# Kernel optimization log

Hardware: AMD Instinct MI355X
Metric: run time of the kernel (lower is better)

The kernel has to match this reference:

```python
import jax, jax.numpy as jnp
import numpy as np

D_MODEL, D_K, D_V, HEADS = 512, 8, 8, 6
EPS = 1e-5


def setup_inputs() -> dict:
    key = jax.random.key(0)
    ks = jax.random.split(key, 16)
    B, S = 16, 1024
    inp = {
        'q_input': jax.random.normal(ks[0], (B, S, D_MODEL), jnp.float32),
        'k_input': jax.random.normal(ks[1], (B, S, D_MODEL), jnp.float32),
        'v_input': jax.random.normal(ks[2], (B, S, D_MODEL), jnp.float32),
        'mask': jax.random.randint(ks[3], (B, S, S), 0, 2).astype(bool),
        'Wq': jax.random.normal(ks[4], (D_MODEL, D_K * HEADS), jnp.float32) * 0.04,
        'bq': jax.random.normal(ks[5], (D_K * HEADS,), jnp.float32) * 0.02,
        'Wk': jax.random.normal(ks[6], (D_MODEL, D_K * HEADS), jnp.float32) * 0.04,
        'bk': jax.random.normal(ks[7], (D_K * HEADS,), jnp.float32) * 0.02,
        'Wv': jax.random.normal(ks[8], (D_MODEL, D_V * HEADS), jnp.float32) * 0.04,
        'bv': jax.random.normal(ks[9], (D_V * HEADS,), jnp.float32) * 0.02,
        'Wo': jax.random.normal(ks[10], (HEADS * D_K, D_MODEL), jnp.float32) * 0.1,
        'bo': jax.random.normal(ks[11], (D_MODEL,), jnp.float32) * 0.02,
        'ln_w': 1.0 + jax.random.normal(ks[12], (D_MODEL,), jnp.float32) * 0.02,
        'ln_b': jax.random.normal(ks[13], (D_MODEL,), jnp.float32) * 0.02,
    }
    return inp


def reference(q_input, k_input, v_input, mask, Wq, bq, Wk, bk, Wv, bv, Wo, bo, ln_w, ln_b):
    B, S, _ = q_input.shape
    # projections -> [B, H, S, d]
    q_s = (q_input @ Wq + bq).reshape(B, S, HEADS, D_K).transpose(0, 2, 1, 3)
    k_s = (k_input @ Wk + bk).reshape(B, S, HEADS, D_K).transpose(0, 2, 1, 3)
    v_s = (v_input @ Wv + bv).reshape(B, S, HEADS, D_V).transpose(0, 2, 1, 3)
    # scaled dot-product with masked_fill(mask, 1e-9) as in the original (fills VALUE, not -inf)
    scores = jnp.einsum('bhqd,bhkd->bhqk', q_s, k_s) / np.sqrt(D_K).astype(np.float32)
    scores = jnp.where(mask[:, None, :, :], jnp.float32(1e-9), scores)
    attn = jax.nn.softmax(scores, axis=-1)
    out = jnp.einsum('bhqk,bhkd->bhqd', attn, v_s)  # [B,H,S,d_v]
    out = out.transpose(0, 2, 1, 3).reshape(B, S, HEADS * D_K)
    out = out @ Wo + bo
    x = q_input + out  # residual
    mu = jnp.mean(x, axis=-1, keepdims=True)
    var = jnp.var(x, axis=-1, keepdims=True)
    return (x - mu) * jax.lax.rsqrt(var + EPS) * ln_w + ln_b
```

## Files before the change

### kernel.cpp

```cpp
#include <hip/hip_runtime.h>

constexpr int B = 16;
constexpr int S = 1024;
constexpr int DM = 512;
constexpr int H = 6;
constexpr int DK = 8;
constexpr int NJ = H * DK;
constexpr int BS = B * S;
constexpr int WB_ELEMS = 16 * NJ * 32;

typedef __attribute__((ext_vector_type(8))) short bf16x8;
typedef __attribute__((ext_vector_type(8))) _Float16 half8;
typedef __attribute__((ext_vector_type(4))) _Float16 half4;
typedef __attribute__((ext_vector_type(4))) float floatx4;

#define LOG2E 1.4426950408889634f
#define QSCALE (0.35355339059327373f * LOG2E)

__device__ inline ushort f2bf(float f) {
  unsigned int u = __builtin_bit_cast(unsigned int, f);
  return (ushort)((u + 0x7FFFu + ((u >> 16) & 1u)) >> 16);
}

__global__ __launch_bounds__(256) void maskbits_kernel(
    const int* __restrict__ mask, unsigned long long* __restrict__ bits) {
  int wave = threadIdx.x >> 6, lane = threadIdx.x & 63;
  int row = blockIdx.x * 4 + wave;
  const int* mrow = mask + (size_t)row * S;
  unsigned long long* brow = bits + (size_t)row * 16;
  int koff = ((lane >> 5) << 5) + 2 * (lane & 15) + ((lane >> 4) & 1);
#pragma unroll
  for (int c = 0; c < 16; c++) {
    int v = mrow[c * 64 + koff];
    unsigned long long bal = __ballot(v != 0);
    if (lane == 0) brow[c] = bal;
  }
}

__global__ __launch_bounds__(256) void wprep_kernel(
    const float* __restrict__ Wq, const float* __restrict__ Wk,
    const float* __restrict__ Wv, ushort* __restrict__ Wb,
    uint2* __restrict__ VBf) {
  int m = blockIdx.x;
  if (m < 3) {
    const float* W = (m == 0) ? Wq : (m == 1) ? Wk : Wv;
    ushort* dst = Wb + (size_t)m * WB_ELEMS;
    for (int e = threadIdx.x; e < WB_ELEMS; e += 256) {
      int kc = e / 1536;
      int rem = e - kc * 1536;
      int n = rem >> 5, kj = rem & 31;
      dst[e] = f2bf(W[(size_t)(kc * 32 + kj) * NJ + n]);
    }
  } else {
    int bh = m - 3;
    for (int i = threadIdx.x; i < 2048; i += 256) {
      int tile = i >> 5;
      int li = i & 31;
      int g = li >> 3, dd = 8 + (li & 7);
      uint hv = (dd == 8) ? 0x3C003C00u : 0u;
      uint2 val; val.x = hv; val.y = hv;
      VBf[((size_t)bh * 64 + tile) * 64 + g * 16 + dd] = val;
    }
  }
}

__global__ __launch_bounds__(256) void proj_kernel(
    const float* __restrict__ q_in, const float* __restrict__ k_in,
    const float* __restrict__ v_in, const ushort* __restrict__ Wb,
    const float* __restrict__ bq, const float* __restrict__ bk,
    const float* __restrict__ bv,
    ushort* __restrict__ Qo, ushort* __restrict__ Ko, ushort* __restrict__ Vo) {
  int m = blockIdx.y;
  const float* x    = (m == 0) ? q_in : (m == 1) ? k_in : v_in;
  const float* bias = (m == 0) ? bq   : (m == 1) ? bk   : bv;
  ushort* out       = (m == 0) ? Qo   : (m == 1) ? Ko   : Vo;
  float oscale      = (m == 0) ? QSCALE : 1.0f;
  const ushort* Wg  = Wb + (size_t)m * WB_ELEMS;

  __shared__ ushort Wl[WB_ELEMS];

  int t = threadIdx.x;
  int r0 = blockIdx.x * 64;
  int wave = t >> 6, lane = t & 63;
  int n16 = lane & 15, quad = lane >> 4;
  const float* xrow = x + (size_t)(r0 + wave * 16 + n16) * DM + quad * 8;

  float4 pa[4], pb[4];
#pragma unroll
  for (int i = 0; i < 4; i++) {
    pa[i] = *(const float4*)(xrow + i * 32);
    pb[i] = *(const float4*)(xrow + i * 32 + 4);
  }

  {
    const uint4* src = (const uint4*)Wg;
    uint4* dst = (uint4*)Wl;
#pragma unroll
    for (int i = 0; i < 12; i++) dst[t + i * 256] = src[t + i * 256];
  }

  floatx4 acc0 = {0.f, 0.f, 0.f, 0.f};
  floatx4 acc1 = {0.f, 0.f, 0.f, 0.f};
  floatx4 acc2 = {0.f, 0.f, 0.f, 0.f};

  __syncthreads();

#pragma unroll
  for (int kc = 0; kc < 16; kc++) {
    float4 xa = pa[kc & 3];
    float4 xb = pb[kc & 3];
    if (kc + 4 < 16) {
      pa[kc & 3] = *(const float4*)(xrow + (kc + 4) * 32);
      pb[kc & 3] = *(const float4*)(xrow + (kc + 4) * 32 + 4);
    }
    bf16x8 a;
    a[0] = (short)f2bf(xa.x); a[1] = (short)f2bf(xa.y);
    a[2] = (short)f2bf(xa.z); a[3] = (short)f2bf(xa.w);
    a[4] = (short)f2bf(xb.x); a[5] = (short)f2bf(xb.y);
    a[6] = (short)f2bf(xb.z); a[7] = (short)f2bf(xb.w);
    const ushort* wbase = &Wl[(kc * 48 + n16) * 32 + quad * 8];
    bf16x8 b0 = *(const bf16x8*)(wbase);
    bf16x8 b1 = *(const bf16x8*)(wbase + 16 * 32);
    bf16x8 b2 = *(const bf16x8*)(wbase + 32 * 32);
    acc0 = __builtin_amdgcn_mfma_f32_16x16x32_bf16(a, b0, acc0, 0, 0, 0);
    acc1 = __builtin_amdgcn_mfma_f32_16x16x32_bf16(a, b1, acc1, 0, 0, 0);
    acc2 = __builtin_amdgcn_mfma_f32_16x16x32_bf16(a, b2, acc2, 0, 0, 0);
  }

  int baseR = r0 + wave * 16 + quad * 4;
#pragma unroll
  for (int j = 0; j < 3; j++) {
    floatx4 a = (j == 0) ? acc0 : (j == 1) ? acc1 : acc2;
    int n = j * 16 + n16;
    float bn = bias[n];
    int h = n >> 3, d = n & 7;
#pragma unroll
    for (int r = 0; r < 4; r++) {
      int R = baseR + r;
      int b = R >> 10, s = R & 1023;
      float fv = (a[r] + bn) * oscale;
      if (m == 2) {
        size_t idx =
            ((((size_t)(b * H + h) * 64 + (s >> 4)) * 64) +
             ((s >> 2) & 3) * 16 + d) * 4 + (s & 3);
        out[idx] = __builtin_bit_cast(ushort, (_Float16)fv);
      } else {
        out[(((size_t)(b * H + h)) * S + s) * 8 + d] = f2bf(fv);
      }
    }
  }
}

__global__ __launch_bounds__(256, 3) void attn_kernel(
    const ushort* __restrict__ Qg, const ushort* __restrict__ Kg,
    const ushort* __restrict__ VBg ,
    const uint* __restrict__ bits32, float* __restrict__ A) {
  int bh = blockIdx.x >> 4;
  int qt = blockIdx.x & 15;
  int b = bh / H, h = bh % H;
  int q0 = qt * 64;

  __shared__ uint4 Kl[1024];
  __shared__ uint2 Vl[64 * 64];

  int t = threadIdx.x;
  int wave = t >> 6, lane = t & 63;
  int quad = lane >> 4, n16 = lane & 15;

  {
    const uint4* Ksrc = (const uint4*)(Kg + (size_t)bh * S * 8);
#pragma unroll
    for (int i = 0; i < 4; i++) Kl[t + i * 256] = Ksrc[t + i * 256];
    const uint2* Vsrc = (const uint2*)VBg + (size_t)bh * (64 * 64);
#pragma unroll
    for (int i = 0; i < 16; i++) Vl[t + i * 256] = Vsrc[t + i * 256];
  }

  bf16x8 aq = {0, 0, 0, 0, 0, 0, 0, 0};
  if (quad == 0)
    aq = *(const bf16x8*)&Qg[((size_t)bh * S + q0 + wave * 16 + n16) * 8];

  const uint* mrow = bits32 + (size_t)(b * S + q0 + wave * 16 + n16) * 32;

  __syncthreads();

  floatx4 acc0 = {0.f, 0.f, 0.f, 0.f};
  floatx4 acc1 = {0.f, 0.f, 0.f, 0.f};
  const floatx4 zero = {0.f, 0.f, 0.f, 0.f};
  int sh0 = 2 * quad;

  const ushort* kb = (const ushort*)Kl + n16 * 8;
  const uint2* vbb = Vl + lane;

#pragma unroll
  for (int cc = 0; cc < 8; cc++) {
    uint4 mq = *(const uint4*)(mrow + cc * 4);
#pragma unroll
    for (int ci = 0; ci < 4; ci++) {
      int c = cc * 4 + ci;
      uint mw = (ci == 0) ? mq.x : (ci == 1) ? mq.y : (ci == 2) ? mq.z : mq.w;

      bf16x8 ak0 = *(const bf16x8*)(kb + c * 256);
      bf16x8 ak1 = *(const bf16x8*)(kb + c * 256 + 128);
      uint2 vb0 = vbb[(2 * c) * 64];
      uint2 vb1 = vbb[(2 * c + 1) * 64];

      floatx4 s0 = __builtin_amdgcn_mfma_f32_16x16x32_bf16(ak0, aq, zero, 0, 0, 0);
      floatx4 s1 = __builtin_amdgcn_mfma_f32_16x16x32_bf16(ak1, aq, zero, 0, 0, 0);

      float p0 = exp2f(fminf(s0[0], 15.f)), p1 = exp2f(fminf(s0[1], 15.f));
      float p2 = exp2f(fminf(s0[2], 15.f)), p3 = exp2f(fminf(s0[3], 15.f));
      float p4 = exp2f(fminf(s1[0], 15.f)), p5 = exp2f(fminf(s1[1], 15.f));
      float p6 = exp2f(fminf(s1[2], 15.f)), p7 = exp2f(fminf(s1[3], 15.f));
      uint w0 = __builtin_bit_cast(uint, __builtin_amdgcn_cvt_pkrtz(p0, p1));
      uint w1 = __builtin_bit_cast(uint, __builtin_amdgcn_cvt_pkrtz(p2, p3));
      uint w2 = __builtin_bit_cast(uint, __builtin_amdgcn_cvt_pkrtz(p4, p5));
      uint w3 = __builtin_bit_cast(uint, __builtin_amdgcn_cvt_pkrtz(p6, p7));

      uint m0 = ((mw >> sh0) & 0x10001u) * 0xFFFFu;
      uint m1 = ((mw >> (sh0 + 1)) & 0x10001u) * 0xFFFFu;
      uint m2 = ((mw >> (sh0 + 8)) & 0x10001u) * 0xFFFFu;
      uint m3 = ((mw >> (sh0 + 9)) & 0x10001u) * 0xFFFFu;
      w0 = (m0 & 0x3C003C00u) | (~m0 & w0);
      w1 = (m1 & 0x3C003C00u) | (~m1 & w1);
      w2 = (m2 & 0x3C003C00u) | (~m2 & w2);
      w3 = (m3 & 0x3C003C00u) | (~m3 & w3);

      uint2 pu0; pu0.x = w0; pu0.y = w1;
      uint2 pu1; pu1.x = w2; pu1.y = w3;
      half4 pa0 = __builtin_bit_cast(half4, pu0);
      half4 pa1 = __builtin_bit_cast(half4, pu1);

      acc0 = __builtin_amdgcn_mfma_f32_16x16x16f16(
          pa0, __builtin_bit_cast(half4, vb0), acc0, 0, 0, 0);
      acc1 = __builtin_amdgcn_mfma_f32_16x16x16f16(
          pa1, __builtin_bit_cast(half4, vb1), acc1, 0, 0, 0);
    }
  }

#pragma unroll
  for (int r = 0; r < 4; r++) {
    float sum = acc0[r] + acc1[r];
    float dnm = __shfl(sum, (lane & 48) | 8, 64);
    if (n16 < 8) {
      int qg = q0 + wave * 16 + quad * 4 + r;
      A[((size_t)(b * S + qg)) * NJ + h * 8 + n16] = sum / dnm;
    }
  }
}

__global__ __launch_bounds__(256) void out_ln_kernel(
    const float* __restrict__ A, const float* __restrict__ Wo,
    const float* __restrict__ bo, const float* __restrict__ qin,
    const float* __restrict__ lnw, const float* __restrict__ lnb,
    float* __restrict__ out) {
  int r0 = blockIdx.x * 8;
  int t = threadIdx.x;
  __shared__ float As[8 * NJ];
#pragma unroll
  for (int i = t; i < 8 * NJ; i += 256) As[i] = A[(size_t)r0 * NJ + i];
  __syncthreads();

  int c0 = t, c1 = t + 256;
  float acc0[8], acc1[8];
#pragma unroll
  for (int r = 0; r < 8; r++) { acc0[r] = 0.f; acc1[r] = 0.f; }

#pragma unroll 4
  for (int j = 0; j < NJ; j++) {
    float w0 = Wo[(size_t)j * DM + c0];
    float w1 = Wo[(size_t)j * DM + c1];
#pragma unroll
    for (int r = 0; r < 8; r++) {
      float a = As[r * NJ + j];
      acc0[r] += a * w0;
      acc1[r] += a * w1;
    }
  }

  float b0 = bo[c0], b1 = bo[c1];
  float y0[8], y1[8], ssum[8], sq[8];
#pragma unroll
  for (int r = 0; r < 8; r++) {
    y0[r] = acc0[r] + b0 + qin[(size_t)(r0 + r) * DM + c0];
    y1[r] = acc1[r] + b1 + qin[(size_t)(r0 + r) * DM + c1];
    ssum[r] = y0[r] + y1[r];
    sq[r] = y0[r] * y0[r] + y1[r] * y1[r];
  }

  int wave = t >> 6, lane = t & 63;
  __shared__ float reds[4][8], redq[4][8];
#pragma unroll
  for (int r = 0; r < 8; r++) {
    float s = ssum[r], qq = sq[r];
#pragma unroll
    for (int off = 32; off > 0; off >>= 1) {
      s += __shfl_xor(s, off, 64);
      qq += __shfl_xor(qq, off, 64);
    }
    if (lane == 0) { reds[wave][r] = s; redq[wave][r] = qq; }
  }
  __syncthreads();

  float lw0 = lnw[c0], lw1 = lnw[c1], lb0 = lnb[c0], lb1 = lnb[c1];
#pragma unroll
  for (int r = 0; r < 8; r++) {
    float s = (reds[0][r] + reds[1][r]) + (reds[2][r] + reds[3][r]);
    float qq = (redq[0][r] + redq[1][r]) + (redq[2][r] + redq[3][r]);
    float mu = s * (1.f / 512.f);
    float var = qq * (1.f / 512.f) - mu * mu;
    float rstd = rsqrtf(var + 1e-5f);
    out[(size_t)(r0 + r) * DM + c0] = (y0[r] - mu) * rstd * lw0 + lb0;
    out[(size_t)(r0 + r) * DM + c1] = (y1[r] - mu) * rstd * lw1 + lb1;
  }
}

extern "C" void kernel_launch(void* const* d_in, const int* in_sizes, int n_in,
                              void* d_out, int out_size, void* d_ws,
                              size_t ws_size, hipStream_t stream) {
  const float* q_in = (const float*)d_in[0];
  const float* k_in = (const float*)d_in[1];
  const float* v_in = (const float*)d_in[2];
  const int* mask = (const int*)d_in[3];
  const float* Wq = (const float*)d_in[4];
  const float* bq = (const float*)d_in[5];
  const float* Wk = (const float*)d_in[6];
  const float* bk = (const float*)d_in[7];
  const float* Wv = (const float*)d_in[8];
  const float* bv = (const float*)d_in[9];
  const float* Wo = (const float*)d_in[10];
  const float* bo = (const float*)d_in[11];
  const float* lnw = (const float*)d_in[12];
  const float* lnb = (const float*)d_in[13];
  float* out = (float*)d_out;

  constexpr size_t QKV = (size_t)B * H * S * DK;
  ushort* base = (ushort*)d_ws;
  ushort* Qw = base;
  ushort* Kw = base + QKV;
  ushort* VBw = base + 2 * QKV;
  float* Aw = (float*)(base + 4 * QKV);
  unsigned long long* bits = (unsigned long long*)(Aw + (size_t)BS * NJ);
  ushort* Wb = (ushort*)(bits + (size_t)BS * 16);

  maskbits_kernel<<<BS / 4, 256, 0, stream>>>(mask, bits);
  wprep_kernel<<<3 + B * H, 256, 0, stream>>>(Wq, Wk, Wv, Wb, (uint2*)VBw);
  proj_kernel<<<dim3(BS / 64, 3), 256, 0, stream>>>(
      q_in, k_in, v_in, Wb, bq, bk, bv, Qw, Kw, VBw);
  attn_kernel<<<(B * H * S) / 64, 256, 0, stream>>>(
      Qw, Kw, VBw, (const uint*)bits, Aw);
  out_ln_kernel<<<BS / 8, 256, 0, stream>>>(Aw, Wo, bo, q_in, lnw, lnb, out);
}
```

Measured before the change: 307.5 us.

## Stage activations in swizzled LDS as bf16 and read weights from global

The projection kernel now loads a 32-row activation tile with coalesced float4 reads, converts it to bf16 once, and stores it in LDS with an XOR swizzle to avoid bank conflicts. The weight matrix is no longer copied to LDS; MFMA B operands are read straight from global memory, relying on L1/L2 caching. Blocks shrink to 128 threads covering 32 rows, which doubles the grid. This removes the per-block 48KB weight copy and the strided per-lane activation reads, at the cost of repeated global weight fetches and losing the register prefetch pipeline.

```diff
diff --git a/kernel.cpp b/kernel.cpp
--- a/kernel.cpp
+++ b/kernel.cpp
@@ -64,7 +64,7 @@
   }
 }
 
-__global__ __launch_bounds__(256) void proj_kernel(
+__global__ __launch_bounds__(128) void proj_kernel(
     const float* __restrict__ q_in, const float* __restrict__ k_in,
     const float* __restrict__ v_in, const ushort* __restrict__ Wb,
     const float* __restrict__ bq, const float* __restrict__ bk,
@@ -77,26 +77,28 @@
   float oscale      = (m == 0) ? QSCALE : 1.0f;
   const ushort* Wg  = Wb + (size_t)m * WB_ELEMS;
 
-  __shared__ ushort Wl[WB_ELEMS];
+  __shared__ ushort Xl[32 * DM];
 
   int t = threadIdx.x;
-  int r0 = blockIdx.x * 64;
+  int r0 = blockIdx.x * 32;
   int wave = t >> 6, lane = t & 63;
   int n16 = lane & 15, quad = lane >> 4;
-  const float* xrow = x + (size_t)(r0 + wave * 16 + n16) * DM + quad * 8;
-
-  float4 pa[4], pb[4];
-#pragma unroll
-  for (int i = 0; i < 4; i++) {
-    pa[i] = *(const float4*)(xrow + i * 32);
-    pb[i] = *(const float4*)(xrow + i * 32 + 4);
-  }
 
   {
-    const uint4* src = (const uint4*)Wg;
-    uint4* dst = (uint4*)Wl;
-#pragma unroll
-    for (int i = 0; i < 12; i++) dst[t + i * 256] = src[t + i * 256];
+    const float4* xs = (const float4*)(x + (size_t)r0 * DM);
+    char* xb = (char*)Xl;
+#pragma unroll 8
+    for (int i = 0; i < 32; i++) {
+      int f4 = t + (i << 7);
+      float4 v = xs[f4];
+      int r = f4 >> 7;
+      int c = (f4 & 127) << 2;
+      ushort4 hv;
+      hv.x = f2bf(v.x); hv.y = f2bf(v.y);
+      hv.z = f2bf(v.z); hv.w = f2bf(v.w);
+      int off = ((r << 10) | (c << 1)) ^ ((r & 7) << 4);
+      *(ushort4*)(xb + off) = hv;
+    }
   }
 
   floatx4 acc0 = {0.f, 0.f, 0.f, 0.f};
@@ -105,20 +107,13 @@
 
   __syncthreads();
 
+  int rr = wave * 16 + n16;
+  const char* xrd = (const char*)Xl;
 #pragma unroll
   for (int kc = 0; kc < 16; kc++) {
-    float4 xa = pa[kc & 3];
-    float4 xb = pb[kc & 3];
-    if (kc + 4 < 16) {
-      pa[kc & 3] = *(const float4*)(xrow + (kc + 4) * 32);
-      pb[kc & 3] = *(const float4*)(xrow + (kc + 4) * 32 + 4);
-    }
-    bf16x8 a;
-    a[0] = (short)f2bf(xa.x); a[1] = (short)f2bf(xa.y);
-    a[2] = (short)f2bf(xa.z); a[3] = (short)f2bf(xa.w);
-    a[4] = (short)f2bf(xb.x); a[5] = (short)f2bf(xb.y);
-    a[6] = (short)f2bf(xb.z); a[7] = (short)f2bf(xb.w);
-    const ushort* wbase = &Wl[(kc * 48 + n16) * 32 + quad * 8];
+    int off = ((rr << 10) | (kc << 6) | (quad << 4)) ^ ((n16 & 7) << 4);
+    bf16x8 a = *(const bf16x8*)(xrd + off);
+    const ushort* wbase = Wg + (kc * 48 + n16) * 32 + quad * 8;
     bf16x8 b0 = *(const bf16x8*)(wbase);
     bf16x8 b1 = *(const bf16x8*)(wbase + 16 * 32);
     bf16x8 b2 = *(const bf16x8*)(wbase + 32 * 32);
@@ -345,7 +340,7 @@
 
   maskbits_kernel<<<BS / 4, 256, 0, stream>>>(mask, bits);
   wprep_kernel<<<3 + B * H, 256, 0, stream>>>(Wq, Wk, Wv, Wb, (uint2*)VBw);
-  proj_kernel<<<dim3(BS / 64, 3), 256, 0, stream>>>(
+  proj_kernel<<<dim3(BS / 32, 3), 128, 0, stream>>>(
       q_in, k_in, v_in, Wb, bq, bk, bv, Qw, Kw, VBw);
   attn_kernel<<<(B * H * S) / 64, 256, 0, stream>>>(
       Qw, Kw, VBw, (const uint*)bits, Aw);
```

New measurement: 317.9 us. 3.4% more time.
